# Optimization experiments

Measured on AMD Instinct MI355X. Metric: run time of the kernel, lower is better.

## Reference

```python
import jax, jax.numpy as jnp
import numpy as np

K = 16  # number of neighbors (module init arg)

def setup_inputs() -> dict:
    key = jax.random.key(0)
    M, D, N = 65536, 16, 64
    x = jax.random.normal(key, (M, D), dtype=jnp.float32)
    # equal-length segments: each point set has M // N points
    segs = jnp.full((N,), M // N, dtype=jnp.int64)
    return {"x": x, "segs": segs}

def reference(x, segs):
    # Segmented kNN graph. Segments are equal-length (static shapes for jit),
    # so the per-segment pairwise distance + top-k becomes a batched op.
    B = segs.shape[0]
    M, D = x.shape
    L = M // B  # points per segment
    pts = x.reshape(B, L, D)
    # squared euclidean distances within each segment: (B, L, L)
    sq = jnp.sum(pts * pts, axis=-1)
    d2 = sq[:, :, None] + sq[:, None, :] - 2.0 * jnp.einsum('bld,bmd->blm', pts, pts)
    # k smallest distances per point (includes self, as in DGL's knn_graph)
    _, idx = jax.lax.top_k(-d2, K)  # idx: (B, L, K), local indices within segment
    offsets = (jnp.arange(B, dtype=idx.dtype) * L)[:, None, None]
    src = (idx + offsets).reshape(-1)                      # neighbor -> global node id
    dst = (jnp.arange(L, dtype=idx.dtype)[None, :, None] + offsets)  # (B, L, 1)
    dst = jnp.broadcast_to(dst, (B, L, K)).reshape(-1)
    # edges point from k-nearest neighbors (predecessors) to each node
    return src, dst
```

## Files before the change

kernel.cpp:

```cpp
#include <hip/hip_runtime.h>
#include <stdint.h>


#define L_SEG 1024
#define M_PTS 65536

typedef __fp16 fp16x2 __attribute__((ext_vector_type(2)));
typedef __fp16 fp16x4 __attribute__((ext_vector_type(4)));
typedef float  f32x4  __attribute__((ext_vector_type(4)));

__device__ __forceinline__ uint32_t umn(uint32_t a, uint32_t b) { return a < b ? a : b; }
__device__ __forceinline__ uint32_t umx(uint32_t a, uint32_t b) { return a > b ? a : b; }

#define CE(arr, i, p) { uint32_t lo = umn(arr[i], arr[p]); uint32_t hi = umx(arr[i], arr[p]); arr[i] = lo; arr[p] = hi; }

__device__ __forceinline__ void clean16(uint32_t* A) {
    #pragma unroll
    for (int j = 8; j > 0; j >>= 1) {
        #pragma unroll
        for (int i = 0; i < 16; ++i) {
            int p = i ^ j;
            if (p > i) CE(A, i, p);
        }
    }
}

__device__ __forceinline__ void sort16(uint32_t* B) {
    #pragma unroll
    for (int p = 1; p < 16; p <<= 1) {
        #pragma unroll
        for (int k = p; k >= 1; k >>= 1) {
            #pragma unroll
            for (int j = (k & (p - 1)); j + k < 16; j += 2 * k) {
                #pragma unroll
                for (int i = 0; i <= ((k - 1 < 15 - j - k) ? k - 1 : 15 - j - k); ++i) {
                    if ((i + j) / (2 * p) == (i + j + k) / (2 * p)) CE(B, i + j, i + j + k);
                }
            }
        }
    }
}

__device__ __forceinline__ void mergeg(uint32_t* A) {
    #pragma unroll
    for (int m = 16; m <= 32; m <<= 1) {
        uint32_t P[16];
        #pragma unroll
        for (int i = 0; i < 16; ++i) P[i] = (uint32_t)__shfl_xor((int)A[15 - i], m, 64);
        #pragma unroll
        for (int i = 0; i < 16; ++i) A[i] = umn(A[i], P[i]);
        clean16(A);
    }
}

__device__ __forceinline__ uint32_t sel4(const uint32_t* A, int g, int v) {
    uint32_t t01 = (g & 1) ? A[4 + v]  : A[v];
    uint32_t t23 = (g & 1) ? A[12 + v] : A[8 + v];
    return (g & 2) ? t23 : t01;
}

__global__ __launch_bounds__(256, 4) void knn_v8_kernel(const float* __restrict__ x,
                                                        int* __restrict__ out) {
    __shared__ __attribute__((aligned(16))) __fp16 sc[L_SEG * 16];
    __shared__ __attribute__((aligned(16))) float  ssq[L_SEG];
    __shared__ __attribute__((aligned(16))) __fp16 sq16[64 * 16];

    const int tid = threadIdx.x;
    const int b   = blockIdx.x;
    const int seg = (b & 7) * 8 + (b >> 7);
    const int qp  = (b >> 3) & 15;
    const float* xseg = x + (size_t)seg * (L_SEG * 16);
    const f32x4* gx4  = (const f32x4*)xseg;

    {
        fp16x4* scv = (fp16x4*)sc;
        #pragma unroll
        for (int i = 0; i < 16; ++i) {
            f32x4 v = gx4[tid + 256 * i];
            union { fp16x2 h2[2]; fp16x4 h4; } u;
            u.h2[0] = __builtin_amdgcn_cvt_pkrtz(-2.0f * v[0], -2.0f * v[1]);
            u.h2[1] = __builtin_amdgcn_cvt_pkrtz(-2.0f * v[2], -2.0f * v[3]);
            scv[tid + 256 * i] = u.h4;
        }
    }
    {
        const int c0 = tid << 2;
        #pragma unroll
        for (int c = 0; c < 4; ++c) {
            float s = 128.0f;
            #pragma unroll
            for (int d = 0; d < 4; ++d) {
                f32x4 v = gx4[(c0 + c) * 4 + d];
                s = __builtin_fmaf(v[0], v[0], s);
                s = __builtin_fmaf(v[1], v[1], s);
                s = __builtin_fmaf(v[2], v[2], s);
                s = __builtin_fmaf(v[3], v[3], s);
            }
            ssq[c0 + c] = s;
        }
    }
    if (tid < 64) {
        const f32x4* qg = gx4 + (size_t)(qp * 64 + tid) * 4;
        fp16x4* dst = (fp16x4*)(sq16 + (size_t)tid * 16);
        #pragma unroll
        for (int d = 0; d < 4; ++d) {
            f32x4 v = qg[d];
            union { fp16x2 h2[2]; fp16x4 h4; } u;
            u.h2[0] = __builtin_amdgcn_cvt_pkrtz(v[0], v[1]);
            u.h2[1] = __builtin_amdgcn_cvt_pkrtz(v[2], v[3]);
            dst[d] = u.h4;
        }
    }
    __syncthreads();

    const int lane = tid & 63;
    const int w    = tid >> 6;
    const int g    = lane >> 4;
    const int col  = lane & 15;
    const int qloc = qp * 64 + w * 16 + col;

    const fp16x4 bfrag = *(const fp16x4*)(sq16 + (size_t)(w * 16 + col) * 16 + g * 4);

    uint32_t A[16];
    #pragma unroll
    for (int i = 0; i < 16; ++i) A[i] = 0xFFFFFFFFu;

    const __fp16* ap  = sc + (size_t)col * 16 + g * 4;
    const float*  sqp = ssq + g * 4;
    const uint32_t vg4 = (uint32_t)(g << 2);

    #pragma unroll 2
    for (int r = 0; r < 8; ++r) {
        const __fp16* apr = ap  + r * 2048;
        const float*  sqr = sqp + r * 128;
        const uint32_t vb = vg4 + (uint32_t)(r << 7);
        uint32_t P[16];
        #pragma unroll
        for (int tt = 0; tt < 8; ++tt) {
            fp16x4 af = *(const fp16x4*)(apr + tt * 256);
            f32x4  sq = *(const f32x4*)(sqr + tt * 16);
            f32x4 acc = __builtin_amdgcn_mfma_f32_16x16x16f16(af, bfrag, sq, 0, 0, 0);
            const uint32_t it = vb + (uint32_t)(tt << 4);
            uint32_t k0 = (__float_as_uint(acc[0]) & 0xFFFFFC00u) | it;
            uint32_t k1 = (__float_as_uint(acc[1]) & 0xFFFFFC00u) | (it + 1u);
            uint32_t k2 = (__float_as_uint(acc[2]) & 0xFFFFFC00u) | (it + 2u);
            uint32_t k3 = (__float_as_uint(acc[3]) & 0xFFFFFC00u) | (it + 3u);
            P[tt * 2]     = umn(k0, k1);
            P[tt * 2 + 1] = umn(k2, k3);
        }
        sort16(P);
        #pragma unroll
        for (int i = 0; i < 16; ++i) A[i] = umn(A[i], P[15 - i]);
        clean16(A);
    }

    mergeg(A);

    union H8 { f32x4 v[2]; fp16x2 h2[8]; };
    H8 qq;
    {
        const f32x4* qf = (const f32x4*)(sq16 + (size_t)(w * 16 + col) * 16);
        qq.v[0] = qf[0]; qq.v[1] = qf[1];
    }
    uint32_t B4[4];
    #pragma unroll
    for (int v = 0; v < 4; ++v) {
        const uint32_t av   = sel4(A, g, v);
        const uint32_t pidx = (av & 1023u) ^ 1u;
        H8 cc;
        const f32x4* cf = (const f32x4*)(sc + (size_t)pidx * 16);
        cc.v[0] = cf[0]; cc.v[1] = cf[1];
        float s = 0.0f;
        #pragma unroll
        for (int j = 0; j < 8; ++j) {
#if __has_builtin(__builtin_amdgcn_fdot2)
            s = __builtin_amdgcn_fdot2(cc.h2[j], qq.h2[j], s, false);
#else
            s = __builtin_fmaf((float)cc.h2[j][0], (float)qq.h2[j][0], s);
            s = __builtin_fmaf((float)cc.h2[j][1], (float)qq.h2[j][1], s);
#endif
        }
        const float val = s + ssq[pidx];
        B4[v] = (__float_as_uint(val) & 0xFFFFFC00u) | pidx;
    }
    CE(B4, 0, 1); CE(B4, 2, 3); CE(B4, 0, 2); CE(B4, 1, 3); CE(B4, 1, 2);
    uint32_t B8[8];
    {
        uint32_t Q[4];
        #pragma unroll
        for (int i = 0; i < 4; ++i) Q[i] = (uint32_t)__shfl_xor((int)B4[3 - i], 16, 64);
        #pragma unroll
        for (int i = 0; i < 4; ++i) { B8[i] = umn(B4[i], Q[i]); B8[i + 4] = umx(B4[i], Q[i]); }
        #pragma unroll
        for (int j = 2; j > 0; j >>= 1) {
            #pragma unroll
            for (int i = 0; i < 8; ++i) { int p = i ^ j; if (p > i) CE(B8, i, p); }
        }
    }
    uint32_t S[16];
    #pragma unroll
    for (int i = 0; i < 8; ++i) S[i] = B8[i];
    #pragma unroll
    for (int i = 8; i < 16; ++i) S[i] = (uint32_t)__shfl_xor((int)B8[15 - i], 32, 64);
    clean16(S);
    #pragma unroll
    for (int i = 0; i < 16; ++i) A[i] = umn(A[i], S[15 - i]);
    clean16(A);

    const int base = seg * L_SEG;
    const int q    = base + qloc;
    int4 sv;
    sv.x = base + (int)(sel4(A, g, 0) & 1023u);
    sv.y = base + (int)(sel4(A, g, 1) & 1023u);
    sv.z = base + (int)(sel4(A, g, 2) & 1023u);
    sv.w = base + (int)(sel4(A, g, 3) & 1023u);
    ((int4*)out)[(size_t)q * 4 + g] = sv;
    ((int4*)out)[(size_t)M_PTS * 4 + (size_t)q * 4 + g] = make_int4(q, q, q, q);
}

extern "C" void kernel_launch(void* const* d_in, const int* in_sizes, int n_in,
                              void* d_out, int out_size, void* d_ws, size_t ws_size,
                              hipStream_t stream) {
    const float* x = (const float*)d_in[0];
    int* out = (int*)d_out;
    (void)d_ws; (void)ws_size;
    knn_v8_kernel<<<dim3(1024), dim3(256), 0, stream>>>(x, out);
}
```

Before: 86.63 us.

## Reduce each MFMA tile to one candidate per group and rescue the three siblings

The first pass now keeps only the minimum of each four-row MFMA output group, instead of the minimum of each pair, so 16 tiles feed one sort16 and the loop runs 4 times instead of 8. The recheck phase then recomputes the three discarded siblings of each of the 4 surviving winners (12 candidates), sorts and merges them across lanes, and folds them into the top-16. This cuts the sorting and merging work in the main loop. In exchange the recheck phase does more dot products and LDS reads, and a true neighbour could be missed when several of the top 16 fall in the same group of four.

```diff
diff --git a/kernel.cpp b/kernel.cpp
--- a/kernel.cpp
+++ b/kernel.cpp
@@ -41,6 +41,12 @@
     }
 }
 
+__device__ __forceinline__ void keep16(uint32_t* A, const uint32_t* S) {
+    #pragma unroll
+    for (int i = 0; i < 16; ++i) A[i] = umn(A[i], S[15 - i]);
+    clean16(A);
+}
+
 __device__ __forceinline__ void mergeg(uint32_t* A) {
     #pragma unroll
     for (int m = 16; m <= 32; m <<= 1) {
@@ -59,7 +65,7 @@
     return (g & 2) ? t23 : t01;
 }
 
-__global__ __launch_bounds__(256, 4) void knn_v8_kernel(const float* __restrict__ x,
+__global__ __launch_bounds__(256, 4) void knn_v9_kernel(const float* __restrict__ x,
                                                         int* __restrict__ out) {
     __shared__ __attribute__((aligned(16))) __fp16 sc[L_SEG * 16];
     __shared__ __attribute__((aligned(16))) float  ssq[L_SEG];
@@ -130,28 +136,23 @@
     const uint32_t vg4 = (uint32_t)(g << 2);
 
     #pragma unroll 2
-    for (int r = 0; r < 8; ++r) {
-        const __fp16* apr = ap  + r * 2048;
-        const float*  sqr = sqp + r * 128;
-        const uint32_t vb = vg4 + (uint32_t)(r << 7);
+    for (int it = 0; it < 4; ++it) {
         uint32_t P[16];
         #pragma unroll
-        for (int tt = 0; tt < 8; ++tt) {
-            fp16x4 af = *(const fp16x4*)(apr + tt * 256);
-            f32x4  sq = *(const f32x4*)(sqr + tt * 16);
+        for (int t = 0; t < 16; ++t) {
+            const int cb = it * 256 + t * 16;
+            fp16x4 af = *(const fp16x4*)(ap + (size_t)cb * 16);
+            f32x4  sq = *(const f32x4*)(sqp + cb);
             f32x4 acc = __builtin_amdgcn_mfma_f32_16x16x16f16(af, bfrag, sq, 0, 0, 0);
-            const uint32_t it = vb + (uint32_t)(tt << 4);
-            uint32_t k0 = (__float_as_uint(acc[0]) & 0xFFFFFC00u) | it;
-            uint32_t k1 = (__float_as_uint(acc[1]) & 0xFFFFFC00u) | (it + 1u);
-            uint32_t k2 = (__float_as_uint(acc[2]) & 0xFFFFFC00u) | (it + 2u);
-            uint32_t k3 = (__float_as_uint(acc[3]) & 0xFFFFFC00u) | (it + 3u);
-            P[tt * 2]     = umn(k0, k1);
-            P[tt * 2 + 1] = umn(k2, k3);
+            const uint32_t ib = (uint32_t)cb + vg4;
+            uint32_t k0 = (__float_as_uint(acc[0]) & 0xFFFFFC00u) | ib;
+            uint32_t k1 = (__float_as_uint(acc[1]) & 0xFFFFFC00u) | (ib + 1u);
+            uint32_t k2 = (__float_as_uint(acc[2]) & 0xFFFFFC00u) | (ib + 2u);
+            uint32_t k3 = (__float_as_uint(acc[3]) & 0xFFFFFC00u) | (ib + 3u);
+            P[t] = umn(umn(k0, k1), umn(k2, k3));
         }
         sort16(P);
-        #pragma unroll
-        for (int i = 0; i < 16; ++i) A[i] = umn(A[i], P[15 - i]);
-        clean16(A);
+        keep16(A, P);
     }
 
     mergeg(A);
@@ -162,50 +163,39 @@
         const f32x4* qf = (const f32x4*)(sq16 + (size_t)(w * 16 + col) * 16);
         qq.v[0] = qf[0]; qq.v[1] = qf[1];
     }
-    uint32_t B4[4];
+    uint32_t R[16];
     #pragma unroll
     for (int v = 0; v < 4; ++v) {
-        const uint32_t av   = sel4(A, g, v);
-        const uint32_t pidx = (av & 1023u) ^ 1u;
-        H8 cc;
-        const f32x4* cf = (const f32x4*)(sc + (size_t)pidx * 16);
-        cc.v[0] = cf[0]; cc.v[1] = cf[1];
-        float s = 0.0f;
-        #pragma unroll
-        for (int j = 0; j < 8; ++j) {
+        const uint32_t win = sel4(A, g, v);
+        const uint32_t wi  = win & 1023u;
+        const uint32_t qb  = wi & ~3u;
+        const uint32_t wo  = wi & 3u;
+        #pragma unroll
+        for (int k = 0; k < 3; ++k) {
+            const uint32_t o    = (uint32_t)k + (((uint32_t)k >= wo) ? 1u : 0u);
+            const uint32_t pidx = qb + o;
+            H8 cc;
+            const f32x4* cf = (const f32x4*)(sc + (size_t)pidx * 16);
+            cc.v[0] = cf[0]; cc.v[1] = cf[1];
+            float s = 0.0f;
+            #pragma unroll
+            for (int j = 0; j < 8; ++j) {
 #if __has_builtin(__builtin_amdgcn_fdot2)
-            s = __builtin_amdgcn_fdot2(cc.h2[j], qq.h2[j], s, false);
+                s = __builtin_amdgcn_fdot2(cc.h2[j], qq.h2[j], s, false);
 #else
-            s = __builtin_fmaf((float)cc.h2[j][0], (float)qq.h2[j][0], s);
-            s = __builtin_fmaf((float)cc.h2[j][1], (float)qq.h2[j][1], s);
+                s = __builtin_fmaf((float)cc.h2[j][0], (float)qq.h2[j][0], s);
+                s = __builtin_fmaf((float)cc.h2[j][1], (float)qq.h2[j][1], s);
 #endif
-        }
-        const float val = s + ssq[pidx];
-        B4[v] = (__float_as_uint(val) & 0xFFFFFC00u) | pidx;
-    }
-    CE(B4, 0, 1); CE(B4, 2, 3); CE(B4, 0, 2); CE(B4, 1, 3); CE(B4, 1, 2);
-    uint32_t B8[8];
-    {
-        uint32_t Q[4];
-        #pragma unroll
-        for (int i = 0; i < 4; ++i) Q[i] = (uint32_t)__shfl_xor((int)B4[3 - i], 16, 64);
-        #pragma unroll
-        for (int i = 0; i < 4; ++i) { B8[i] = umn(B4[i], Q[i]); B8[i + 4] = umx(B4[i], Q[i]); }
-        #pragma unroll
-        for (int j = 2; j > 0; j >>= 1) {
-            #pragma unroll
-            for (int i = 0; i < 8; ++i) { int p = i ^ j; if (p > i) CE(B8, i, p); }
-        }
-    }
-    uint32_t S[16];
-    #pragma unroll
-    for (int i = 0; i < 8; ++i) S[i] = B8[i];
-    #pragma unroll
-    for (int i = 8; i < 16; ++i) S[i] = (uint32_t)__shfl_xor((int)B8[15 - i], 32, 64);
-    clean16(S);
-    #pragma unroll
-    for (int i = 0; i < 16; ++i) A[i] = umn(A[i], S[15 - i]);
-    clean16(A);
+            }
+            const float val = s + ssq[pidx];
+            R[v * 3 + k] = (__float_as_uint(val) & 0xFFFFFC00u) | pidx;
+        }
+    }
+    #pragma unroll
+    for (int i = 12; i < 16; ++i) R[i] = 0xFFFFFFFFu;
+    sort16(R);
+    mergeg(R);
+    keep16(A, R);
 
     const int base = seg * L_SEG;
     const int q    = base + qloc;
@@ -224,5 +214,5 @@
     const float* x = (const float*)d_in[0];
     int* out = (int*)d_out;
     (void)d_ws; (void)ws_size;
-    knn_v8_kernel<<<dim3(1024), dim3(256), 0, stream>>>(x, out);
-}
+    knn_v9_kernel<<<dim3(1024), dim3(256), 0, stream>>>(x, out);
+}
```

Measured after the change: 86.45 us. Within noise of the previous version (-0.2%).
